# Kernel tuning notes

Hardware: AMD Instinct MI355X
Metric: run time of the kernel (lower is better)

## Reference

```python
import jax, jax.numpy as jnp
import numpy as np

N_LAYERS = 4
B, L, D = 2, 2048, 512
H, E = 8, 64          # n_heads = d_model // d_head
DFF = 1024
EPS = 1e-6
MAX_LOG_SCALE = float(np.log(100.0))   # QKNorm max_scale clamp
LOG10 = float(np.log(10.0))            # QKNorm scale init


def rms_norm(x, scale, eps=EPS):
    # matches torch rms_norm: x * (scale * rsqrt(mean(x^2, -1) + eps))
    ms = jnp.mean(jnp.square(x), axis=-1, keepdims=True)
    return x * (scale * jax.lax.rsqrt(ms + eps))


def rope(x):
    # standard rotary embedding over head dim, half-split convention. x: [n,h,l,e]
    e, l = x.shape[-1], x.shape[-2]
    inv = 1.0 / (10000.0 ** (jnp.arange(0, e, 2, dtype=jnp.float32) / e))
    freqs = jnp.arange(l, dtype=jnp.float32)[:, None] * inv[None, :]   # [l, e/2]
    cos, sin = jnp.cos(freqs), jnp.sin(freqs)
    x1, x2 = x[..., : e // 2], x[..., e // 2:]
    return jnp.concatenate([x1 * cos - x2 * sin, x1 * sin + x2 * cos], axis=-1)


def setup_inputs() -> dict:
    key = jax.random.key(0)
    ks = jax.random.split(key, 10)
    s = 0.02
    return {
        "x": jax.random.normal(ks[0], (B, L, D), jnp.float32),
        "cond": jax.random.normal(ks[1], (B, D), jnp.float32),
        "attn_mask": jnp.ones((B, L), jnp.int32),
        # per-layer stacked params (torch Linear(in,out,bias=False) stored as [in,out], y = x @ W)
        "wn_attn": s * jax.random.normal(ks[2], (N_LAYERS, D, D), jnp.float32),      # AdaRMSNorm cond proj (attn)
        "wqkv": s * jax.random.normal(ks[3], (N_LAYERS, D, 3 * D), jnp.float32),
        "qk_scale": jnp.full((N_LAYERS, H), LOG10, jnp.float32),                     # QKNorm per-head log-scale
        "wout": s * jax.random.normal(ks[4], (N_LAYERS, D, D), jnp.float32),
        "wn_ff": s * jax.random.normal(ks[5], (N_LAYERS, D, D), jnp.float32),        # AdaRMSNorm cond proj (ff)
        "wup": s * jax.random.normal(ks[6], (N_LAYERS, D, 2 * DFF), jnp.float32),
        "wdown": s * jax.random.normal(ks[7], (N_LAYERS, DFF, D), jnp.float32),
        "out_scale": jnp.ones((D,), jnp.float32),                                    # final RMSNorm scale
    }


def forward(x, cond, attn_mask, wn_attn, wqkv, qk_scale, wout, wn_ff, wup, wdown, out_scale):
    n, l, d = x.shape
    # mask bias: (attn_mask != 1) * -1e9, repeated 'n l -> n h l s' (query-dim mask, as in source)
    bias = (attn_mask != 1).astype(x.dtype) * -1e9
    bias = bias[:, None, :, None]  # [n,1,l,1] broadcast over heads and key dim

    def block(h_x, p):
        wn_a, w_qkv, qs, w_o, wn_f, w_up, w_dn = p
        # --- self attention ---
        skip = h_x
        y = rms_norm(h_x, (cond @ wn_a + 1.0)[:, None, :])            # AdaRMSNorm
        qkv = y @ w_qkv                                               # [n,l,3d]
        q, k, v = jnp.split(qkv, 3, axis=-1)
        to_heads = lambda t: t.reshape(n, l, H, E).transpose(0, 2, 1, 3)
        q, k, v = to_heads(q), to_heads(k), to_heads(v)
        qs_c = jnp.minimum(qs, MAX_LOG_SCALE)
        hs = jnp.exp(0.5 * qs_c - 0.25 * np.log(E))[:, None, None]    # [H,1,1] QKNorm scale
        q = rope(rms_norm(q, hs))
        k = rope(rms_norm(k, hs))
        scores = jnp.einsum('nhle,nhse->nhls', q, k) / np.sqrt(E) + bias
        attn = jax.nn.softmax(scores, axis=-1)
        o = jnp.einsum('nhls,nhse->nhle', attn, v)
        o = o.transpose(0, 2, 1, 3).reshape(n, l, d)
        h_x = skip + o @ w_o
        # --- GEGLU feed-forward ---
        skip = h_x
        y = rms_norm(h_x, (cond @ wn_f + 1.0)[:, None, :])
        u = y @ w_up
        a, b = jnp.split(u, 2, axis=-1)
        y = a * jax.nn.gelu(b, approximate=False)                     # F.gelu exact
        h_x = skip + y @ w_dn
        return h_x, None

    x, _ = jax.lax.scan(block, x, (wn_attn, wqkv, qk_scale, wout, wn_ff, wup, wdown))
    return rms_norm(x, out_scale)


def reference(x, cond, attn_mask, wn_attn, wqkv, qk_scale, wout, wn_ff, wup, wdown, out_scale):
    return forward(x, cond, attn_mask, wn_attn, wqkv, qk_scale, wout, wn_ff, wup, wdown, out_scale)
```

## Files before the change

kernel.cpp:

```cpp
#include <hip/hip_runtime.h>
#include <hip/hip_bf16.h>

#define NB 2
#define LL 2048
#define DD 512
#define HH 8
#define EE 64
#define DFF 1024
#define NL 4
#define EPS_F 1e-6f

typedef __bf16 bf16x8 __attribute__((ext_vector_type(8)));
typedef __bf16 bf16x4 __attribute__((ext_vector_type(4)));
typedef float f32x4 __attribute__((ext_vector_type(4)));

__device__ __forceinline__ unsigned short f2bf(float f) {
    unsigned int u = __float_as_uint(f);
    unsigned int r = (u + 0x7FFFu + ((u >> 16) & 1u)) >> 16;
    return (unsigned short)r;
}
__device__ __forceinline__ unsigned short f2bf_t(float f) {
    return (unsigned short)(__float_as_uint(f) >> 16);
}
__device__ __forceinline__ void gload16(const void* g, void* l) {
    __builtin_amdgcn_global_load_lds(
        (const __attribute__((address_space(1))) unsigned int*)g,
        (__attribute__((address_space(3))) unsigned int*)l, 16, 0, 0);
}

__global__ void rope_table_kernel(float* __restrict__ cosT, float* __restrict__ sinT) {
    int idx = blockIdx.x * 256 + threadIdx.x;
    if (idx >= LL * 32) return;
    int l = idx >> 5, i = idx & 31;
    float inv = powf(10000.f, -(float)i * (1.f / 32.f));
    float ang = (float)l * inv;
    cosT[idx] = cosf(ang);
    sinT[idx] = sinf(ang);
}

__global__ __launch_bounds__(256) void wcast_all_kernel(const float* __restrict__ wqkv,
                                                        const float* __restrict__ wout,
                                                        const float* __restrict__ wup,
                                                        const float* __restrict__ wdown,
                                                        unsigned short* __restrict__ wt) {
    int bid = blockIdx.x;
    int layer = bid / 2560, rem = bid % 2560;
    const float* W; unsigned short* WT; int K, N, t;
    if (rem < 768)       { W = wqkv  + (size_t)layer * 786432;  WT = wt + (size_t)layer * 786432;            K = 512;  N = 1536; t = rem; }
    else if (rem < 1024) { W = wout  + (size_t)layer * 262144;  WT = wt + 3145728 + (size_t)layer * 262144;  K = 512;  N = 512;  t = rem - 768; }
    else if (rem < 2048) { W = wup   + (size_t)layer * 1048576; WT = wt + 4194304 + (size_t)layer * 1048576; K = 512;  N = 2048; t = rem - 1024; }
    else                 { W = wdown + (size_t)layer * 524288;  WT = wt + 8388608 + (size_t)layer * 524288;  K = 1024; N = 512;  t = rem - 2048; }
    int tn = N / 32;
    int n0 = (t % tn) * 32, k0 = (t / tn) * 32;
    __shared__ float tile[32][33];
    int r = threadIdx.x >> 5, c = threadIdx.x & 31;
#pragma unroll
    for (int i = 0; i < 4; ++i)
        tile[r + 8 * i][c] = W[(size_t)(k0 + r + 8 * i) * N + n0 + c];
    __syncthreads();
#pragma unroll
    for (int i = 0; i < 4; ++i)
        WT[(size_t)(n0 + r + 8 * i) * K + k0 + c] = f2bf(tile[c][r + 8 * i]);
}

__global__ __launch_bounds__(256) void cond_all_kernel(const float* __restrict__ cond,
                                                       const float* __restrict__ wn_attn,
                                                       const float* __restrict__ wn_ff,
                                                       float* __restrict__ s_all) {
    int bid = blockIdx.x;
    int d0 = (bid & 7) * 64;
    int b = (bid >> 3) & 1;
    int which = (bid >> 4) & 1;
    int layer = bid >> 5;
    const float* W = (which ? wn_ff : wn_attn) + (size_t)layer * DD * DD;
    int t = threadIdx.x;
    int d = d0 + (t & 63), kq = t >> 6;
    const float* c = cond + b * DD + kq * 128;
    const float* Wp = W + (size_t)(kq * 128) * DD + d;
    float s = 0.f;
#pragma unroll 8
    for (int j = 0; j < 128; ++j) s = fmaf(c[j], Wp[(size_t)j * DD], s);
    __shared__ float red[4][64];
    red[kq][t & 63] = s;
    __syncthreads();
    if (t < 64) {
        float tot = 1.f + red[0][t] + red[1][t] + red[2][t] + red[3][t];
        s_all[((size_t)(layer * 2 + which) * NB + b) * DD + d0 + t] = tot;
    }
}

__global__ __launch_bounds__(256) void rmsnorm_bf16_kernel(const float* __restrict__ x,
                                                           const float* __restrict__ scale,
                                                           unsigned short* __restrict__ y) {
    int row = blockIdx.x;
    int b = row >> 11;
    int t = threadIdx.x;
    float2 v = ((const float2*)(x + (size_t)row * DD))[t];
    float ss = v.x * v.x + v.y * v.y;
#pragma unroll
    for (int o = 32; o > 0; o >>= 1) ss += __shfl_xor(ss, o);
    __shared__ float red[4];
    if ((t & 63) == 0) red[t >> 6] = ss;
    __syncthreads();
    float tot = red[0] + red[1] + red[2] + red[3];
    float inv = rsqrtf(tot * (1.f / DD) + EPS_F);
    float2 s2 = ((const float2*)(scale + b * DD))[t];
    unsigned int lo = f2bf(v.x * s2.x * inv);
    unsigned int hi = f2bf(v.y * s2.y * inv);
    ((unsigned int*)(y + (size_t)row * DD))[t] = lo | (hi << 16);
}

__global__ __launch_bounds__(256) void rmsnorm_f32_kernel(const float* __restrict__ x,
                                                          const float* __restrict__ scale,
                                                          float* __restrict__ y) {
    int row = blockIdx.x;
    int t = threadIdx.x;
    float2 v = ((const float2*)(x + (size_t)row * DD))[t];
    float ss = v.x * v.x + v.y * v.y;
#pragma unroll
    for (int o = 32; o > 0; o >>= 1) ss += __shfl_xor(ss, o);
    __shared__ float red[4];
    if ((t & 63) == 0) red[t >> 6] = ss;
    __syncthreads();
    float tot = red[0] + red[1] + red[2] + red[3];
    float inv = rsqrtf(tot * (1.f / DD) + EPS_F);
    float2 s2 = ((const float2*)scale)[t];
    float2 o2;
    o2.x = v.x * s2.x * inv;
    o2.y = v.y * s2.y * inv;
    ((float2*)(y + (size_t)row * DD))[t] = o2;
}

template <int BN>
__global__ __launch_bounds__(256) void gemm_bf16_kernel(const unsigned short* __restrict__ A,
                                                        const unsigned short* __restrict__ BT,
                                                        const float* __restrict__ R,
                                                        float* __restrict__ C,
                                                        int M, int N, int K) {
    constexpr int NJ = BN / 32;
    __shared__ __align__(16) unsigned short As[2][128 * 32];
    __shared__ __align__(16) unsigned short Bs[2][BN * 32];
    int tid = threadIdx.x;
    int n0 = blockIdx.x * BN, m0 = blockIdx.y * 128;
    int w = tid >> 6, l = tid & 63;
    int wr = w >> 1, wc = w & 1;
    int kf = 8 * (l >> 4);
    int rf = l & 15;

    auto stage = [&](int buf, int k0) {
#pragma unroll
        for (int u = 0; u < 2; ++u) {
            int c = u * 256 + tid;
            int row = c >> 2, ch = c & 3;
            gload16(A + (size_t)(m0 + row) * K + k0 + ch * 8, &As[buf][c * 8]);
        }
#pragma unroll
        for (int u = 0; u < BN / 64; ++u) {
            int c = u * 256 + tid;
            int row = c >> 2, ch = c & 3;
            gload16(BT + (size_t)(n0 + row) * K + k0 + ch * 8, &Bs[buf][c * 8]);
        }
    };

    f32x4 acc[4][NJ] = {};
    const int nt = K / 32;
    stage(0, 0);
    __syncthreads();

    for (int t = 0; t < nt; ++t) {
        if (t + 1 < nt) stage((t + 1) & 1, (t + 1) * 32);
        int cur = t & 1;
        bf16x8 a[4], b[NJ];
#pragma unroll
        for (int i = 0; i < 4; ++i)
            a[i] = *(const bf16x8*)(&As[cur][(wr * 64 + i * 16 + rf) * 32 + kf]);
#pragma unroll
        for (int j = 0; j < NJ; ++j)
            b[j] = *(const bf16x8*)(&Bs[cur][(wc * (BN / 2) + j * 16 + rf) * 32 + kf]);
#pragma unroll
        for (int i = 0; i < 4; ++i)
#pragma unroll
            for (int j = 0; j < NJ; ++j)
                acc[i][j] = __builtin_amdgcn_mfma_f32_16x16x32_bf16(a[i], b[j], acc[i][j], 0, 0, 0);
        __syncthreads();
    }

    int rl = l >> 4, cl = l & 15;
#pragma unroll
    for (int i = 0; i < 4; ++i)
#pragma unroll
        for (int j = 0; j < NJ; ++j)
#pragma unroll
            for (int r = 0; r < 4; ++r) {
                int row = m0 + wr * 64 + i * 16 + rl * 4 + r;
                int col = n0 + wc * (BN / 2) + j * 16 + cl;
                size_t off = (size_t)row * N + col;
                float v = acc[i][j][r];
                if (R) v += R[off];
                C[off] = v;
            }
}

__global__ __launch_bounds__(256) void gemm_qkv_fused_kernel(const unsigned short* __restrict__ A,
                                                             const unsigned short* __restrict__ BT,
                                                             const float* __restrict__ qs,
                                                             const float* __restrict__ cosT,
                                                             const float* __restrict__ sinT,
                                                             unsigned short* __restrict__ qh,
                                                             unsigned short* __restrict__ kh,
                                                             unsigned short* __restrict__ vt) {
    __shared__ __align__(16) unsigned char smem[128 * 65 * sizeof(float)];
    unsigned short* As = (unsigned short*)smem;
    unsigned short* Bs = (unsigned short*)(smem + 16384);
    float* ex = (float*)smem;
    int tid = threadIdx.x;
    int ct = blockIdx.x, m0 = blockIdx.y * 128;
    int n0 = ct * 64;
    int w = tid >> 6, l = tid & 63;
    int wr = w >> 1, wc = w & 1;
    int kf = 8 * (l >> 4);
    int rf = l & 15;

    auto stage = [&](int buf, int k0) {
#pragma unroll
        for (int u = 0; u < 2; ++u) {
            int c = u * 256 + tid;
            int row = c >> 2, ch = c & 3;
            gload16(A + (size_t)(m0 + row) * DD + k0 + ch * 8, &As[buf * 4096 + c * 8]);
        }
        int c = tid;
        int row = c >> 2, ch = c & 3;
        gload16(BT + (size_t)(n0 + row) * DD + k0 + ch * 8, &Bs[buf * 2048 + c * 8]);
    };

    f32x4 acc[4][2] = {};
    stage(0, 0);
    __syncthreads();
    for (int t = 0; t < 16; ++t) {
        if (t + 1 < 16) stage((t + 1) & 1, (t + 1) * 32);
        int cur = t & 1;
        bf16x8 a[4], b[2];
#pragma unroll
        for (int i = 0; i < 4; ++i)
            a[i] = *(const bf16x8*)(&As[cur * 4096 + (wr * 64 + i * 16 + rf) * 32 + kf]);
#pragma unroll
        for (int j = 0; j < 2; ++j)
            b[j] = *(const bf16x8*)(&Bs[cur * 2048 + (wc * 32 + j * 16 + rf) * 32 + kf]);
#pragma unroll
        for (int i = 0; i < 4; ++i)
#pragma unroll
            for (int j = 0; j < 2; ++j)
                acc[i][j] = __builtin_amdgcn_mfma_f32_16x16x32_bf16(a[i], b[j], acc[i][j], 0, 0, 0);
        __syncthreads();
    }

    int rl = l >> 4, cl = l & 15;
#pragma unroll
    for (int i = 0; i < 4; ++i)
#pragma unroll
        for (int j = 0; j < 2; ++j)
#pragma unroll
            for (int r = 0; r < 4; ++r)
                ex[(wr * 64 + i * 16 + rl * 4 + r) * 65 + wc * 32 + j * 16 + cl] = acc[i][j][r];
    __syncthreads();

    int b = m0 >> 11;
    int lbase = m0 & (LL - 1);
    if (ct < 16) {
        int h = ct & 7;
        bool isq = ct < 8;
        float hsc = expf(0.5f * fminf(qs[h], 4.60517019f) - 1.03972077f) * 0.35355339059f;
        if (isq) hsc *= 1.44269504f;
        unsigned short* dst = (isq ? qh : kh) + ((size_t)(b * HH + h) * LL) * EE;
#pragma unroll 4
        for (int it = 0; it < 32; ++it) {
            int row = w * 32 + it;
            int lloc = lbase + row;
            float v = ex[row * 65 + l];
            float ss = v * v;
#pragma unroll
            for (int d = 1; d < 64; d <<= 1) ss += __shfl_xor(ss, d);
            float inv = hsc * rsqrtf(ss * (1.f / EE) + EPS_F);
            float pr = ex[row * 65 + (l ^ 32)];
            int i2 = l & 31;
            float c = cosT[lloc * 32 + i2], s = sinT[lloc * 32 + i2];
            float vn = v * inv, pn = pr * inv;
            float o = (l < 32) ? (vn * c - pn * s) : (pn * s + vn * c);
            dst[(size_t)lloc * EE + l] = f2bf(o);
        }
    } else {
        int h = ct - 16;
        int bh = b * HH + h;
#pragma unroll 4
        for (int it = 0; it < 16; ++it) {
            int e = w * 16 + it;
            float v0 = ex[(2 * l) * 65 + e];
            float v1 = ex[(2 * l + 1) * 65 + e];
            unsigned int pk = (unsigned int)f2bf(v0) | ((unsigned int)f2bf(v1) << 16);
            *(unsigned int*)(vt + ((size_t)(bh * EE + e)) * LL + lbase + 2 * l) = pk;
        }
    }
}

__global__ __launch_bounds__(256) void gemm_geglu_kernel(const unsigned short* __restrict__ A,
                                                         const unsigned short* __restrict__ BT,
                                                         unsigned short* __restrict__ G) {
    __shared__ __align__(16) unsigned char smem[128 * 65 * sizeof(float)];
    unsigned short* As = (unsigned short*)smem;
    unsigned short* Bs = (unsigned short*)(smem + 16384);
    float* ep = (float*)smem;
    int tid = threadIdx.x;
    int n0 = blockIdx.x * 64, m0 = blockIdx.y * 128;
    int w = tid >> 6, l = tid & 63;
    int wr = w >> 1, wc = w & 1;
    int kf = 8 * (l >> 4);
    int rf = l & 15;

    auto stage = [&](int buf, int k0) {
#pragma unroll
        for (int u = 0; u < 2; ++u) {
            int c = u * 256 + tid;
            int row = c >> 2, ch = c & 3;
            gload16(A + (size_t)(m0 + row) * DD + k0 + ch * 8, &As[buf * 4096 + c * 8]);
            int grow = (row < 64) ? (n0 + row) : (DFF + n0 + row - 64);
            gload16(BT + (size_t)grow * DD + k0 + ch * 8, &Bs[buf * 4096 + c * 8]);
        }
    };

    f32x4 acc[4][4] = {};
    stage(0, 0);
    __syncthreads();

    for (int t = 0; t < 16; ++t) {
        if (t + 1 < 16) stage((t + 1) & 1, (t + 1) * 32);
        int cur = t & 1;
        bf16x8 a[4], b[4];
#pragma unroll
        for (int i = 0; i < 4; ++i)
            a[i] = *(const bf16x8*)(&As[cur * 4096 + (wr * 64 + i * 16 + rf) * 32 + kf]);
#pragma unroll
        for (int j = 0; j < 4; ++j)
            b[j] = *(const bf16x8*)(&Bs[cur * 4096 + (wc * 64 + j * 16 + rf) * 32 + kf]);
#pragma unroll
        for (int i = 0; i < 4; ++i)
#pragma unroll
            for (int j = 0; j < 4; ++j)
                acc[i][j] = __builtin_amdgcn_mfma_f32_16x16x32_bf16(a[i], b[j], acc[i][j], 0, 0, 0);
        __syncthreads();
    }

    int rl = l >> 4, cl = l & 15;
    if (wc == 0) {
#pragma unroll
        for (int i = 0; i < 4; ++i)
#pragma unroll
            for (int j = 0; j < 4; ++j)
#pragma unroll
                for (int r = 0; r < 4; ++r)
                    ep[(wr * 64 + i * 16 + rl * 4 + r) * 65 + j * 16 + cl] = acc[i][j][r];
    }
    __syncthreads();
    if (wc == 1) {
#pragma unroll
        for (int i = 0; i < 4; ++i)
#pragma unroll
            for (int j = 0; j < 4; ++j)
#pragma unroll
                for (int r = 0; r < 4; ++r) {
                    int row = wr * 64 + i * 16 + rl * 4 + r;
                    float bv = acc[i][j][r];
                    float av = ep[row * 65 + j * 16 + cl];
                    float ge = 0.5f * bv * (1.f + erff(bv * 0.70710678f));
                    G[(size_t)(m0 + row) * DFF + n0 + j * 16 + cl] = f2bf(av * ge);
                }
    }
}

#define KVB 32
#define KLDP 72
#define VLDP 40
#define PLDP 36
__global__ __launch_bounds__(256) void flash_mfma_kernel(const unsigned short* __restrict__ qh,
                                                         const unsigned short* __restrict__ kh,
                                                         const unsigned short* __restrict__ vt,
                                                         unsigned short* __restrict__ op,
                                                         float* __restrict__ os) {
    __shared__ unsigned short K_lds[2][32 * KLDP];
    __shared__ unsigned short VT_lds[2][64 * VLDP];
    __shared__ unsigned short S_lds[16 * VLDP];
    __shared__ unsigned short P_lds[4][16 * PLDP];
    int bid = blockIdx.x;
    int qb = bid & 31, h = (bid >> 5) & 7, b = (bid >> 8) & 1, split = bid >> 9;
    int bh = b * HH + h;
    int tid = threadIdx.x, w = tid >> 6, l = tid & 63;
    int lo = l & 15, hi4 = l >> 4;
    int q0 = qb * 64 + w * 16;

    for (int idx = tid; idx < 16 * VLDP; idx += 256) {
        int rr = idx / VLDP;
        S_lds[idx] = (rr == 0) ? 0x3F80 : 0;
    }

    const unsigned short* qbase = qh + ((size_t)bh * LL) * EE;
    bf16x8 qa[2];
#pragma unroll
    for (int s = 0; s < 2; ++s)
        qa[s] = *(const bf16x8*)(qbase + (size_t)(q0 + lo) * EE + s * 32 + 8 * hi4);

    int krow = tid >> 3, kch = tid & 7;
    int vrow = tid >> 2, vch = tid & 3;
    const uint4* gK = (const uint4*)(kh + ((size_t)bh * LL + split * 16 * KVB + krow) * EE + kch * 8);
    const uint4* gV = (const uint4*)(vt + ((size_t)bh * EE + vrow) * LL + split * 16 * KVB + vch * 8);
    const int gKstep = KVB * EE / 8;
    const int gVstep = KVB / 8;
    unsigned short* ldsK = &K_lds[0][krow * KLDP + kch * 8];
    unsigned short* ldsV = &VT_lds[0][vrow * VLDP + vch * 8];
    const int ldsKsz = 32 * KLDP, ldsVsz = 64 * VLDP;

    uint4 pk = *gK, pv = *gV;
    *(uint4*)ldsK = pk;
    *(uint4*)ldsV = pv;
    __syncthreads();

    f32x4 oacc[4] = {};
    f32x4 osum = {};

    for (int t = 0; t < 16; ++t) {
        int cur = t & 1;
        if (t + 1 < 16) {
            pk = gK[(t + 1) * gKstep];
            pv = gV[(t + 1) * gVstep];
        }

        const unsigned short* Kc = &K_lds[cur][0];
        const unsigned short* Vc = &VT_lds[cur][0];
        f32x4 S[2] = {};
        __builtin_amdgcn_s_setprio(1);
#pragma unroll
        for (int nf = 0; nf < 2; ++nf)
#pragma unroll
            for (int s = 0; s < 2; ++s) {
                bf16x8 kb = *(const bf16x8*)&Kc[(nf * 16 + lo) * KLDP + s * 32 + 8 * hi4];
                S[nf] = __builtin_amdgcn_mfma_f32_16x16x32_bf16(qa[s], kb, S[nf], 0, 0, 0);
            }
        __builtin_amdgcn_s_setprio(0);

#pragma unroll
        for (int r = 0; r < 4; ++r)
#pragma unroll
            for (int nf = 0; nf < 2; ++nf)
                P_lds[w][(hi4 * 4 + r) * PLDP + nf * 16 + lo] = f2bf_t(exp2f(S[nf][r]));

        __builtin_amdgcn_s_setprio(1);
        bf16x4 p0 = *(const bf16x4*)&P_lds[w][lo * PLDP + 8 * hi4];
        bf16x4 p1 = *(const bf16x4*)&P_lds[w][lo * PLDP + 8 * hi4 + 4];
        bf16x8 pa;
#pragma unroll
        for (int j = 0; j < 4; ++j) { pa[j] = p0[j]; pa[4 + j] = p1[j]; }
#pragma unroll
        for (int nf = 0; nf < 4; ++nf) {
            bf16x8 vb = *(const bf16x8*)&Vc[(nf * 16 + lo) * VLDP + 8 * hi4];
            oacc[nf] = __builtin_amdgcn_mfma_f32_16x16x32_bf16(pa, vb, oacc[nf], 0, 0, 0);
        }
        bf16x8 vbE = *(const bf16x8*)&S_lds[lo * VLDP + 8 * hi4];
        osum = __builtin_amdgcn_mfma_f32_16x16x32_bf16(pa, vbE, osum, 0, 0, 0);
        __builtin_amdgcn_s_setprio(0);

        if (t + 1 < 16) {
            *(uint4*)(ldsK + (cur ^ 1) * ldsKsz) = pk;
            *(uint4*)(ldsV + (cur ^ 1) * ldsVsz) = pv;
        }
        __syncthreads();
    }

    unsigned short* opp = op + (size_t)split * (NB * LL * DD);
#pragma unroll
    for (int r = 0; r < 4; ++r) {
        int row = q0 + hi4 * 4 + r;
        unsigned short* optr = opp + ((size_t)(b * LL + row)) * DD + h * EE;
#pragma unroll
        for (int nf = 0; nf < 4; ++nf)
            optr[nf * 16 + lo] = f2bf(oacc[nf][r]);
        if (lo == 0)
            os[split * (NB * HH * LL) + bh * LL + row] = osum[r];
    }
}

__global__ __launch_bounds__(256) void attn_combine_kernel(const unsigned short* __restrict__ op,
                                                           const float* __restrict__ os,
                                                           unsigned short* __restrict__ oh) {
    int idx = (blockIdx.x * 256 + threadIdx.x) * 8;
    int col = idx & 511;
    int h = col >> 6;
    int row = (idx >> 9) & (LL - 1);
    int b = idx >> 20;
    int bh = b * HH + h;
    float s = 0.f;
    float a[8] = {};
#pragma unroll
    for (int sp = 0; sp < 4; ++sp) {
        s += os[sp * (NB * HH * LL) + bh * LL + row];
        uint4 t = *(const uint4*)(op + (size_t)sp * (NB * LL * DD) + idx);
        unsigned int dw[4] = {t.x, t.y, t.z, t.w};
#pragma unroll
        for (int j = 0; j < 4; ++j) {
            a[2 * j]     += __uint_as_float(dw[j] << 16);
            a[2 * j + 1] += __uint_as_float(dw[j] & 0xFFFF0000u);
        }
    }
    float inv = 1.f / s;
    uint4 o4;
    unsigned int* po = (unsigned int*)&o4;
#pragma unroll
    for (int j = 0; j < 4; ++j)
        po[j] = (unsigned int)f2bf(a[2 * j] * inv) | ((unsigned int)f2bf(a[2 * j + 1] * inv) << 16);
    *(uint4*)(oh + idx) = o4;
}

extern "C" void kernel_launch(void* const* d_in, const int* in_sizes, int n_in,
                              void* d_out, int out_size, void* d_ws, size_t ws_size,
                              hipStream_t stream) {
    const float* x        = (const float*)d_in[0];
    const float* cond     = (const float*)d_in[1];
    const float* wn_attn  = (const float*)d_in[3];
    const float* wqkv     = (const float*)d_in[4];
    const float* qk_scale = (const float*)d_in[5];
    const float* wout     = (const float*)d_in[6];
    const float* wn_ff    = (const float*)d_in[7];
    const float* wup      = (const float*)d_in[8];
    const float* wdown    = (const float*)d_in[9];
    const float* out_scale= (const float*)d_in[10];
    float* out = (float*)d_out;

    const int TOK = NB * LL;
    const size_t nHx = (size_t)TOK * DD;
    const size_t M = 1024 * 1024;

    float* ws = (float*)d_ws;
    float* hx  = ws;
    unsigned short* y_bf = (unsigned short*)(ws + 2 * M);
    unsigned short* op   = (unsigned short*)(ws + 3 * M);
    unsigned short* qh_bf = (unsigned short*)(ws + 11 * M);
    unsigned short* g_bf  = (unsigned short*)(ws + 11 * M);
    unsigned short* kh_bf = (unsigned short*)(ws + 12 * M);
    unsigned short* vt_bf = (unsigned short*)(ws + 13 * M);
    unsigned short* oh_bf = (unsigned short*)(ws + 14 * M);
    unsigned short* wt = (unsigned short*)(ws + 15 * M);
    float* smal  = ws + 20 * M;
    float* s_all = smal;
    float* os    = smal + 8192;
    float* cosT  = os + 131072;
    float* sinT  = cosT + 65536;

    hipMemcpyAsync(hx, x, nHx * sizeof(float), hipMemcpyDeviceToDevice, stream);
    rope_table_kernel<<<256, 256, 0, stream>>>(cosT, sinT);
    cond_all_kernel<<<128, 256, 0, stream>>>(cond, wn_attn, wn_ff, s_all);
    wcast_all_kernel<<<10240, 256, 0, stream>>>(wqkv, wout, wup, wdown, wt);

    unsigned short* wqkvT  = wt;
    unsigned short* woutT  = wt + 3145728;
    unsigned short* wupT   = wt + 4194304;
    unsigned short* wdownT = wt + 8388608;

    for (int layer = 0; layer < NL; ++layer) {
        const float* qs = qk_scale + layer * HH;

        rmsnorm_bf16_kernel<<<TOK, 256, 0, stream>>>(hx, s_all + (size_t)(layer * 2 + 0) * NB * DD, y_bf);
        gemm_qkv_fused_kernel<<<dim3(24, TOK / 128), 256, 0, stream>>>(
            y_bf, wqkvT + (size_t)layer * 786432, qs, cosT, sinT, qh_bf, kh_bf, vt_bf);
        flash_mfma_kernel<<<2048, 256, 0, stream>>>(qh_bf, kh_bf, vt_bf, op, os);
        attn_combine_kernel<<<1024, 256, 0, stream>>>(op, os, oh_bf);
        gemm_bf16_kernel<64><<<dim3(512 / 64, TOK / 128), 256, 0, stream>>>(
            oh_bf, woutT + (size_t)layer * 262144, hx, hx, TOK, 512, 512);

        rmsnorm_bf16_kernel<<<TOK, 256, 0, stream>>>(hx, s_all + (size_t)(layer * 2 + 1) * NB * DD, y_bf);
        gemm_geglu_kernel<<<dim3(16, 32), 256, 0, stream>>>(
            y_bf, wupT + (size_t)layer * 1048576, g_bf);
        gemm_bf16_kernel<64><<<dim3(512 / 64, TOK / 128), 256, 0, stream>>>(
            g_bf, wdownT + (size_t)layer * 524288, hx, hx, TOK, 512, 1024);
    }
    rmsnorm_f32_kernel<<<TOK, 256, 0, stream>>>(hx, out_scale, out);
}
```

Baseline: 571.9 us.

## Transpose QK MFMA and pass P via cross-lane shuffles instead of LDS

Swaps the MFMA operand order so the score tile comes out transposed, letting each lane hold probabilities for its own query row. The bf16 P operand is then built with packed xor-shuffles instead of a round trip through per-wave LDS. The row sum is now computed with register adds and shuffles, which replaces the extra MFMA against a ones matrix. This removes LDS stores and loads, the ones-matrix setup and one MFMA per tile, at the cost of extra shuffle and select instructions whose lane mapping is intricate and easy to get wrong.

```diff
diff --git a/kernel.cpp b/kernel.cpp
--- a/kernel.cpp
+++ b/kernel.cpp
@@ -11,7 +11,6 @@
 #define EPS_F 1e-6f
 
 typedef __bf16 bf16x8 __attribute__((ext_vector_type(8)));
-typedef __bf16 bf16x4 __attribute__((ext_vector_type(4)));
 typedef float f32x4 __attribute__((ext_vector_type(4)));
 
 __device__ __forceinline__ unsigned short f2bf(float f) {
@@ -19,8 +18,8 @@
     unsigned int r = (u + 0x7FFFu + ((u >> 16) & 1u)) >> 16;
     return (unsigned short)r;
 }
-__device__ __forceinline__ unsigned short f2bf_t(float f) {
-    return (unsigned short)(__float_as_uint(f) >> 16);
+__device__ __forceinline__ unsigned int packbf_t(float a, float b) {
+    return (__float_as_uint(a) >> 16) | (__float_as_uint(b) & 0xFFFF0000u);
 }
 __device__ __forceinline__ void gload16(const void* g, void* l) {
     __builtin_amdgcn_global_load_lds(
@@ -379,7 +378,6 @@
 #define KVB 32
 #define KLDP 72
 #define VLDP 40
-#define PLDP 36
 __global__ __launch_bounds__(256) void flash_mfma_kernel(const unsigned short* __restrict__ qh,
                                                          const unsigned short* __restrict__ kh,
                                                          const unsigned short* __restrict__ vt,
@@ -387,19 +385,12 @@
                                                          float* __restrict__ os) {
     __shared__ unsigned short K_lds[2][32 * KLDP];
     __shared__ unsigned short VT_lds[2][64 * VLDP];
-    __shared__ unsigned short S_lds[16 * VLDP];
-    __shared__ unsigned short P_lds[4][16 * PLDP];
     int bid = blockIdx.x;
     int qb = bid & 31, h = (bid >> 5) & 7, b = (bid >> 8) & 1, split = bid >> 9;
     int bh = b * HH + h;
     int tid = threadIdx.x, w = tid >> 6, l = tid & 63;
     int lo = l & 15, hi4 = l >> 4;
     int q0 = qb * 64 + w * 16;
-
-    for (int idx = tid; idx < 16 * VLDP; idx += 256) {
-        int rr = idx / VLDP;
-        S_lds[idx] = (rr == 0) ? 0x3F80 : 0;
-    }
 
     const unsigned short* qbase = qh + ((size_t)bh * LL) * EE;
     bf16x8 qa[2];
@@ -423,7 +414,11 @@
     __syncthreads();
 
     f32x4 oacc[4] = {};
-    f32x4 osum = {};
+    float rsum = 0.f;
+    const bool lowg = hi4 < 2;
+    const bool oddg = hi4 & 1;
+    const bool topg = hi4 >> 1;
+    const int par = (hi4 ^ (hi4 >> 1)) & 1;
 
     for (int t = 0; t < 16; ++t) {
         int cur = t & 1;
@@ -441,29 +436,38 @@
 #pragma unroll
             for (int s = 0; s < 2; ++s) {
                 bf16x8 kb = *(const bf16x8*)&Kc[(nf * 16 + lo) * KLDP + s * 32 + 8 * hi4];
-                S[nf] = __builtin_amdgcn_mfma_f32_16x16x32_bf16(qa[s], kb, S[nf], 0, 0, 0);
+                S[nf] = __builtin_amdgcn_mfma_f32_16x16x32_bf16(kb, qa[s], S[nf], 0, 0, 0);
             }
         __builtin_amdgcn_s_setprio(0);
 
-#pragma unroll
-        for (int r = 0; r < 4; ++r)
-#pragma unroll
-            for (int nf = 0; nf < 2; ++nf)
-                P_lds[w][(hi4 * 4 + r) * PLDP + nf * 16 + lo] = f2bf_t(exp2f(S[nf][r]));
+        float p0 = exp2f(S[0][0]), p1 = exp2f(S[0][1]), p2 = exp2f(S[0][2]), p3 = exp2f(S[0][3]);
+        float p4 = exp2f(S[1][0]), p5 = exp2f(S[1][1]), p6 = exp2f(S[1][2]), p7 = exp2f(S[1][3]);
+
+        float ts = ((p0 + p1) + (p2 + p3)) + ((p4 + p5) + (p6 + p7));
+        ts += __shfl_xor(ts, 16);
+        ts += __shfl_xor(ts, 32);
+        rsum += ts;
+
+        unsigned int u0 = packbf_t(p0, p1), u1 = packbf_t(p2, p3);
+        unsigned int u2 = packbf_t(p4, p5), u3 = packbf_t(p6, p7);
+        unsigned int keep0 = lowg ? u0 : u2, keep1 = lowg ? u1 : u3;
+        unsigned int sA0 = lowg ? u2 : u0, sA1 = lowg ? u3 : u1;
+        unsigned int rA0 = __shfl_xor(sA0, 32), rA1 = __shfl_xor(sA1, 32);
+        unsigned int sB0 = par ? keep0 : rA0, sB1 = par ? keep1 : rA1;
+        unsigned int rB0 = __shfl_xor(sB0, 16), rB1 = __shfl_xor(sB1, 16);
+        uint4 paw;
+        paw.x = oddg ? rB0 : (topg ? rA0 : keep0);
+        paw.y = oddg ? rB1 : (topg ? rA1 : keep1);
+        paw.z = oddg ? (topg ? keep0 : rA0) : rB0;
+        paw.w = oddg ? (topg ? keep1 : rA1) : rB1;
+        bf16x8 pa = *(bf16x8*)&paw;
 
         __builtin_amdgcn_s_setprio(1);
-        bf16x4 p0 = *(const bf16x4*)&P_lds[w][lo * PLDP + 8 * hi4];
-        bf16x4 p1 = *(const bf16x4*)&P_lds[w][lo * PLDP + 8 * hi4 + 4];
-        bf16x8 pa;
-#pragma unroll
-        for (int j = 0; j < 4; ++j) { pa[j] = p0[j]; pa[4 + j] = p1[j]; }
 #pragma unroll
         for (int nf = 0; nf < 4; ++nf) {
             bf16x8 vb = *(const bf16x8*)&Vc[(nf * 16 + lo) * VLDP + 8 * hi4];
             oacc[nf] = __builtin_amdgcn_mfma_f32_16x16x32_bf16(pa, vb, oacc[nf], 0, 0, 0);
         }
-        bf16x8 vbE = *(const bf16x8*)&S_lds[lo * VLDP + 8 * hi4];
-        osum = __builtin_amdgcn_mfma_f32_16x16x32_bf16(pa, vbE, osum, 0, 0, 0);
         __builtin_amdgcn_s_setprio(0);
 
         if (t + 1 < 16) {
@@ -481,9 +485,9 @@
 #pragma unroll
         for (int nf = 0; nf < 4; ++nf)
             optr[nf * 16 + lo] = f2bf(oacc[nf][r]);
-        if (lo == 0)
-            os[split * (NB * HH * LL) + bh * LL + row] = osum[r];
-    }
+    }
+    if (hi4 == 0)
+        os[split * (NB * HH * LL) + bh * LL + q0 + lo] = rsum;
 }
 
 __global__ __launch_bounds__(256) void attn_combine_kernel(const unsigned short* __restrict__ op,
```

Result: no change. 579.9 us (+1.4%).
